# Kernel tuning notes

Measured on AMD Instinct MI355X. Metric: run time of the kernel, lower is better.

The kernel has to match this reference:

```python
import jax, jax.numpy as jnp
import numpy as np

DIM = 112        # input channels
DIM_OUT = 224    # output channels (stage transition)
HEADS = 4
HD = DIM_OUT // HEADS          # 56
WS = 8                         # window size before query pooling
QS = 2                         # query_stride
MLP_DIM = int(DIM_OUT * 4.0)   # 896
EPS = 1e-6
SCALE = HD ** -0.5


def _layernorm(x, g, b):
    m = x.mean(-1, keepdims=True)
    d = x - m
    v = (d * d).mean(-1, keepdims=True)
    return d * jax.lax.rsqrt(v + EPS) * g + b


def _maxpool2(x):
    # stride==pool_size max pooling via reshape (NHWC)
    B, H, W, C = x.shape
    return x.reshape(B, H // QS, QS, W // QS, QS, C).max(axis=(2, 4))


def setup_inputs() -> dict:
    key = jax.random.key(0)
    ks = jax.random.split(key, 8)
    def n(k, s, sc=0.02):
        return jax.random.normal(k, s, dtype=jnp.float32) * sc
    return {
        "hidden_states": jax.random.normal(ks[0], (8, 128, 128, DIM), dtype=jnp.float32),
        "ln1_g": jnp.ones((DIM,), jnp.float32),
        "ln1_b": jnp.zeros((DIM,), jnp.float32),
        "qkv_w": n(ks[1], (DIM, 3 * DIM_OUT)),
        "qkv_b": jnp.zeros((3 * DIM_OUT,), jnp.float32),
        "attn_proj_w": n(ks[2], (DIM_OUT, DIM_OUT)),
        "attn_proj_b": jnp.zeros((DIM_OUT,), jnp.float32),
        "res_proj_w": n(ks[3], (DIM, DIM_OUT)),
        "res_proj_b": jnp.zeros((DIM_OUT,), jnp.float32),
        "ln2_g": jnp.ones((DIM_OUT,), jnp.float32),
        "ln2_b": jnp.zeros((DIM_OUT,), jnp.float32),
        "mlp1_w": n(ks[4], (DIM_OUT, MLP_DIM)),
        "mlp1_b": jnp.zeros((MLP_DIM,), jnp.float32),
        "mlp2_w": n(ks[5], (MLP_DIM, DIM_OUT)),
        "mlp2_b": jnp.zeros((DIM_OUT,), jnp.float32),
    }


def reference(hidden_states, ln1_g, ln1_b, qkv_w, qkv_b, attn_proj_w, attn_proj_b,
              res_proj_w, res_proj_b, ln2_g, ln2_b, mlp1_w, mlp1_b, mlp2_w, mlp2_b):
    x = hidden_states
    B, H, W, _ = x.shape  # H, W divisible by WS -> no padding branch needed
    hs = _layernorm(x, ln1_g, ln1_b)
    # dim != dim_out: residual = pooled projection of normed input
    residual = _maxpool2(hs @ res_proj_w + res_proj_b)  # (B, H/2, W/2, DIM_OUT)

    # window partition: (B*nh*nw, WS, WS, DIM)
    nh, nw = H // WS, W // WS
    w = hs.reshape(B, nh, WS, nw, WS, DIM).transpose(0, 1, 3, 2, 4, 5)
    w = w.reshape(B * nh * nw, WS, WS, DIM)

    # multi-scale attention with query pooling
    qkv = (w @ qkv_w + qkv_b).reshape(-1, WS * WS, 3, HEADS, HD)
    q, k, v = qkv[:, :, 0], qkv[:, :, 1], qkv[:, :, 2]
    q = _maxpool2(q.reshape(-1, WS, WS, DIM_OUT))          # (Bw, WS/2, WS/2, DIM_OUT)
    q = q.reshape(-1, (WS // QS) ** 2, HEADS, HD)
    q = q.transpose(0, 2, 1, 3)   # (Bw, h, Lq, d)
    k = k.transpose(0, 2, 1, 3)   # (Bw, h, Lk, d)
    v = v.transpose(0, 2, 1, 3)
    attn = jax.nn.softmax(jnp.einsum('bhqd,bhkd->bhqk', q * SCALE, k), axis=-1)
    o = jnp.einsum('bhqk,bhkd->bhqd', attn, v).transpose(0, 2, 1, 3)
    ws2 = WS // QS
    o = o.reshape(-1, ws2, ws2, DIM_OUT)
    o = o @ attn_proj_w + attn_proj_b

    # window unpartition at pooled resolution
    H2, W2 = H // QS, W // QS
    o = o.reshape(B, nh, nw, ws2, ws2, DIM_OUT).transpose(0, 1, 3, 2, 4, 5)
    o = o.reshape(B, H2, W2, DIM_OUT)

    hs = residual + o
    ln = _layernorm(hs, ln2_g, ln2_b)
    mlp = jax.nn.gelu(ln @ mlp1_w + mlp1_b, approximate=False) @ mlp2_w + mlp2_b
    return hs + mlp
```

## Files before the change

### kernel.cpp

```cpp
#include <hip/hip_runtime.h>
#include <hip/hip_bf16.h>
#include <math.h>


#define SCALE_A 0.13363062095621219f

typedef __attribute__((ext_vector_type(8))) short short8;
typedef __attribute__((ext_vector_type(4))) short short4v;
typedef __attribute__((ext_vector_type(4))) float f32x4;
typedef __attribute__((ext_vector_type(16))) float f32x16;

__device__ inline short f2bf(float x) {
  __hip_bfloat16 h = __float2bfloat16(x);
  union { __hip_bfloat16 h; short s; } u; u.h = h;
  return u.s;
}
__device__ inline float gelu_fast(float x) {
  float x2 = x * x;
  float p = fmaf(x2, 0.044715f, 1.0f);
  float t = -1.5957691216057308f * x * p;
  return x / (1.0f + __expf(t));
}

__global__ void cast_w_kernel(const float* __restrict__ qkv_w,
                              const float* __restrict__ rp_w,
                              const float* __restrict__ ap_w,
                              const float* __restrict__ m1_w,
                              const float* __restrict__ m2_w,
                              short* __restrict__ wF) {
  int tid = blockIdx.x * blockDim.x + threadIdx.x;
  int stride = gridDim.x * blockDim.x;
  for (int e = tid; e < 90112; e += stride) {
    int j = e & 7, lr = (e >> 3) & 15, lqq = (e >> 7) & 3, tile = e >> 9;
    int kt = tile & 3, nt = tile >> 2;
    int cp = nt * 16 + lr;
    int h = cp / 176, cl = cp % 176;
    int k = kt * 32 + lqq * 8 + j;
    float val = 0.f;
    if (k < 112 && cl < 168) {
      int bcol = (cl < 56) ? (h * 56 + cl)
               : (cl < 112) ? (224 + h * 56 + (cl - 56))
                            : (448 + h * 56 + (cl - 112));
      val = qkv_w[k * 672 + bcol];
    }
    wF[e] = f2bf(val);
  }
  for (int e = tid; e < 28672; e += stride) {
    int j = e & 7, lr = (e >> 3) & 15, lqq = (e >> 7) & 3, tile = e >> 9;
    int kt = tile & 3, nt = tile >> 2;
    int n = nt * 16 + lr, k = kt * 32 + lqq * 8 + j;
    wF[90112 + e] = (k < 112) ? f2bf(rp_w[k * 224 + n]) : (short)0;
  }
  for (int e = tid; e < 50176; e += stride) {
    int j = e & 7, lr = (e >> 3) & 15, lqq = (e >> 7) & 3, tile = e >> 9;
    int kt = tile % 7, nt = tile / 7;
    int n = nt * 16 + lr, k = kt * 32 + lqq * 8 + j;
    wF[118784 + e] = f2bf(ap_w[k * 224 + n]);
  }
  for (int e = tid; e < 200704; e += stride) {
    int j = e & 7, lane = (e >> 3) & 63, unit = e >> 9;
    int kt = unit % 14, nt = unit / 14;
    int n = nt * 32 + (lane & 31), k = kt * 16 + (lane >> 5) * 8 + j;
    wF[168960 + e] = f2bf(m1_w[k * 896 + n]);
  }
  for (int e = tid; e < 200704; e += stride) {
    int j = e & 7, lane = (e >> 3) & 63, unit = e >> 9;
    int kt = unit % 56, nt = unit / 56;
    int n = nt * 32 + (lane & 31), k = kt * 16 + (lane >> 5) * 8 + j;
    wF[369664 + e] = f2bf(m2_w[k * 224 + n]);
  }
}

__global__ __launch_bounds__(256, 2) void attn_kernel(
    const float* __restrict__ x, const float* __restrict__ ln1_g,
    const float* __restrict__ ln1_b, const short* __restrict__ qkvF,
    const float* __restrict__ qkv_b, const short* __restrict__ apF,
    const float* __restrict__ apb, const short* __restrict__ rpF,
    const float* __restrict__ rpb, float* __restrict__ hs2) {
  __shared__ alignas(16) short u_s[4 * 9792];
  int win = blockIdx.x;
  int nw = win & 15, nh = (win >> 4) & 15, b = win >> 8;
  int tid = threadIdx.x;
  int wave = tid >> 6, lane = tid & 63, lrow = lane & 15, lq = lane >> 4;
  short* w_s  = u_s;
  short* k_s  = u_s + wave * 9792;
  short* vT_s = k_s + 4608;
  short* qp_s = k_s + 8640;

  {
    int part = tid & 3, m = tid >> 2;
    int p = m >> 2, r = m & 3;
    int tr = (p >> 2) * 2 + (r >> 1), tc = (p & 3) * 2 + (r & 1);
    size_t token = ((size_t)(b * 128 + nh * 8 + tr)) * 128 + (nw * 8 + tc);
    const float* xp = x + token * 112 + part * 28;
    f32x4 v[7];
    #pragma unroll
    for (int i = 0; i < 7; ++i) v[i] = *(const f32x4*)(xp + i * 4);
    float s = 0.f;
    #pragma unroll
    for (int i = 0; i < 7; ++i) s += v[i][0] + v[i][1] + v[i][2] + v[i][3];
    s += __shfl_xor(s, 1, 4);
    s += __shfl_xor(s, 2, 4);
    float mean = s * (1.f / 112.f);
    float s2 = 0.f;
    #pragma unroll
    for (int i = 0; i < 7; ++i)
      #pragma unroll
      for (int q = 0; q < 4; ++q) { float d = v[i][q] - mean; s2 = fmaf(d, d, s2); }
    s2 += __shfl_xor(s2, 1, 4);
    s2 += __shfl_xor(s2, 2, 4);
    float rs = rsqrtf(s2 * (1.f / 112.f) + 1e-6f);
    const float* gp = ln1_g + part * 28;
    const float* bp = ln1_b + part * 28;
    #pragma unroll
    for (int i = 0; i < 7; ++i) {
      f32x4 gg = *(const f32x4*)(gp + i * 4);
      f32x4 bb = *(const f32x4*)(bp + i * 4);
      short4v o;
      #pragma unroll
      for (int q = 0; q < 4; ++q)
        o[q] = f2bf((v[i][q] - mean) * rs * gg[q] + bb[q]);
      *(short4v*)&w_s[m * 136 + part * 28 + i * 4] = o;
    }
  }
  if (tid < 192) {
    short8 z = {0, 0, 0, 0, 0, 0, 0, 0};
    *(short8*)&w_s[(tid / 3) * 136 + 112 + (tid % 3) * 8] = z;
  }
  __syncthreads();

  short8 Aw[4][4];
  #pragma unroll
  for (int mt = 0; mt < 4; ++mt)
    #pragma unroll
    for (int kt = 0; kt < 4; ++kt)
      Aw[mt][kt] = *(const short8*)&w_s[(mt * 16 + lrow) * 136 + kt * 32 + lq * 8];
  __syncthreads();

  {
    short8 z = {0, 0, 0, 0, 0, 0, 0, 0};
    *(short8*)&k_s[lane * 72 + 56] = z;
    if (lane < 16) *(short8*)&qp_s[lane * 72 + 56] = z;
  }

  int h = wave;

  #pragma unroll 2
  for (int t = 0; t < 11; ++t) {
    int cl = t * 16 + lrow;
    f32x4 ac[4] = {{0.f,0.f,0.f,0.f},{0.f,0.f,0.f,0.f},
                   {0.f,0.f,0.f,0.f},{0.f,0.f,0.f,0.f}};
    short8 bw[4];
    #pragma unroll
    for (int kt = 0; kt < 4; ++kt)
      bw[kt] = *(const short8*)(qkvF + (((h * 11 + t) * 4 + kt) * 64 + lane) * 8);
    #pragma unroll
    for (int kt = 0; kt < 4; ++kt)
      #pragma unroll
      for (int mt = 0; mt < 4; ++mt)
        ac[mt] = __builtin_amdgcn_mfma_f32_16x16x32_bf16(Aw[mt][kt], bw[kt], ac[mt], 0, 0, 0);
    if (cl < 56) {
      float bias = qkv_b[h * 56 + cl];
      #pragma unroll
      for (int mt = 0; mt < 4; ++mt) {
        float mx = fmaxf(fmaxf(ac[mt][0], ac[mt][1]),
                         fmaxf(ac[mt][2], ac[mt][3])) + bias;
        qp_s[(mt * 4 + lq) * 72 + cl] = f2bf(mx * SCALE_A);
      }
    } else if (cl < 112) {
      float bias = qkv_b[224 + h * 56 + (cl - 56)];
      #pragma unroll
      for (int mt = 0; mt < 4; ++mt)
        #pragma unroll
        for (int r = 0; r < 4; ++r)
          k_s[(mt * 16 + lq * 4 + r) * 72 + (cl - 56)] = f2bf(ac[mt][r] + bias);
    } else if (cl < 168) {
      float bias = qkv_b[448 + h * 56 + (cl - 112)];
      #pragma unroll
      for (int mt = 0; mt < 4; ++mt) {
        short4v pk = {f2bf(ac[mt][0] + bias), f2bf(ac[mt][1] + bias),
                      f2bf(ac[mt][2] + bias), f2bf(ac[mt][3] + bias)};
        *(short4v*)&vT_s[(cl - 112) * 72 + mt * 16 + lq * 4] = pk;
      }
    }
  }

  short8 aq[2];
  #pragma unroll
  for (int kt = 0; kt < 2; ++kt)
    aq[kt] = *(const short8*)&qp_s[lrow * 72 + kt * 32 + lq * 8];
  f32x4 sc[4];
  #pragma unroll
  for (int t = 0; t < 4; ++t) {
    sc[t][0] = sc[t][1] = sc[t][2] = sc[t][3] = 0.f;
    #pragma unroll
    for (int kt = 0; kt < 2; ++kt) {
      short8 bk = *(const short8*)&k_s[(t * 16 + lrow) * 72 + kt * 32 + lq * 8];
      sc[t] = __builtin_amdgcn_mfma_f32_16x16x32_bf16(aq[kt], bk, sc[t], 0, 0, 0);
    }
  }
  float mr[4], sr[4];
  #pragma unroll
  for (int r = 0; r < 4; ++r)
    mr[r] = fmaxf(fmaxf(sc[0][r], sc[1][r]), fmaxf(sc[2][r], sc[3][r]));
  #pragma unroll
  for (int off = 8; off; off >>= 1)
    #pragma unroll
    for (int r = 0; r < 4; ++r) mr[r] = fmaxf(mr[r], __shfl_xor(mr[r], off, 16));
  #pragma unroll
  for (int r = 0; r < 4; ++r) {
    #pragma unroll
    for (int t = 0; t < 4; ++t) sc[t][r] = __expf(sc[t][r] - mr[r]);
    sr[r] = sc[0][r] + sc[1][r] + sc[2][r] + sc[3][r];
  }
  #pragma unroll
  for (int off = 8; off; off >>= 1)
    #pragma unroll
    for (int r = 0; r < 4; ++r) sr[r] += __shfl_xor(sr[r], off, 16);
  #pragma unroll
  for (int r = 0; r < 4; ++r) sr[r] = 1.f / sr[r];
  #pragma unroll
  for (int t = 0; t < 4; ++t)
    #pragma unroll
    for (int r = 0; r < 4; ++r)
      qp_s[(lq * 4 + r) * 72 + t * 16 + lrow] = f2bf(sc[t][r] * sr[r]);

  short8 ap[2];
  #pragma unroll
  for (int kt = 0; kt < 2; ++kt)
    ap[kt] = *(const short8*)&qp_s[lrow * 72 + kt * 32 + lq * 8];
  #pragma unroll
  for (int ct = 0; ct < 4; ++ct) {
    int c0 = (ct < 3) ? ct * 16 : 40;
    int col = c0 + lrow;
    f32x4 ov = {0.f, 0.f, 0.f, 0.f};
    #pragma unroll
    for (int kt = 0; kt < 2; ++kt) {
      short8 bv = *(const short8*)&vT_s[col * 72 + kt * 32 + lq * 8];
      ov = __builtin_amdgcn_mfma_f32_16x16x32_bf16(ap[kt], bv, ov, 0, 0, 0);
    }
    if (ct < 3 || lrow >= 8) {
      #pragma unroll
      for (int r = 0; r < 4; ++r)
        qp_s[(lq * 4 + r) * 72 + col] = f2bf(ov[r]);
    }
  }

  int nt0 = (wave < 2) ? wave * 4 : 8 + (wave - 2) * 3;
  int ncnt2 = (wave < 2) ? 4 : 3;
  float resv[4][4];
  #pragma unroll
  for (int i = 0; i < 4; ++i) {
    if (i < ncnt2) {
      int nt = nt0 + i;
      f32x4 racc[4] = {{0.f,0.f,0.f,0.f},{0.f,0.f,0.f,0.f},
                       {0.f,0.f,0.f,0.f},{0.f,0.f,0.f,0.f}};
      short8 rw[4];
      #pragma unroll
      for (int kt = 0; kt < 4; ++kt)
        rw[kt] = *(const short8*)(rpF + (((nt * 4) + kt) * 64 + lane) * 8);
      #pragma unroll
      for (int kt = 0; kt < 4; ++kt)
        #pragma unroll
        for (int mt = 0; mt < 4; ++mt)
          racc[mt] = __builtin_amdgcn_mfma_f32_16x16x32_bf16(Aw[mt][kt], rw[kt], racc[mt], 0, 0, 0);
      float bi = rpb[nt * 16 + lrow];
      #pragma unroll
      for (int mt = 0; mt < 4; ++mt)
        resv[i][mt] = fmaxf(fmaxf(racc[mt][0], racc[mt][1]),
                            fmaxf(racc[mt][2], racc[mt][3])) + bi;
    }
  }
  __syncthreads();

  float* res_s = (float*)u_s;
  #pragma unroll
  for (int i = 0; i < 4; ++i) {
    if (i < ncnt2) {
      int nt = nt0 + i;
      #pragma unroll
      for (int mt = 0; mt < 4; ++mt)
        res_s[(mt * 4 + lq) * 228 + nt * 16 + lrow] = resv[i][mt];
    }
  }

  short8 Ao[7];
  #pragma unroll
  for (int kt = 0; kt < 7; ++kt) {
    int c = kt * 32 + lq * 8;
    int h2 = (c >= 168) ? 3 : (c >= 112) ? 2 : (c >= 56) ? 1 : 0;
    Ao[kt] = *(const short8*)&u_s[h2 * 9792 + 8640 + lrow * 72 + (c - h2 * 56)];
  }
  for (int i = 0; i < ncnt2; ++i) {
    int nt = nt0 + i;
    f32x4 acc = {0.f, 0.f, 0.f, 0.f};
    #pragma unroll
    for (int kt = 0; kt < 7; ++kt) {
      short8 bw = *(const short8*)(apF + ((nt * 7 + kt) * 64 + lane) * 8);
      acc = __builtin_amdgcn_mfma_f32_16x16x32_bf16(Ao[kt], bw, acc, 0, 0, 0);
    }
    int col2 = nt * 16 + lrow;
    float bi = apb[col2];
    #pragma unroll
    for (int r = 0; r < 4; ++r) {
      float res = res_s[(lq * 4 + r) * 228 + col2];
      size_t token = ((size_t)(b * 64 + nh * 4 + lq)) * 64 + nw * 4 + r;
      hs2[token * 224 + col2] = res + acc[r] + bi;
    }
  }
}

template <int NT>
__device__ __forceinline__ void mlp1_tiles(
    int nt0, const short* ln_s, const short* __restrict__ m1F,
    const float* __restrict__ b1, short* hid_s, int nl, int half, int lane) {
  f32x16 acc[NT];
  #pragma unroll
  for (int i = 0; i < NT; ++i)
    #pragma unroll
    for (int r = 0; r < 16; ++r) acc[i][r] = 0.f;
  #pragma unroll
  for (int kt = 0; kt < 14; ++kt) {
    short8 a = *(const short8*)&ln_s[nl * 232 + kt * 16 + half * 8];
    #pragma unroll
    for (int i = 0; i < NT; ++i) {
      short8 bw = *(const short8*)(m1F + ((size_t)((nt0 + i) * 14 + kt) * 64 + lane) * 8);
      acc[i] = __builtin_amdgcn_mfma_f32_32x32x16_bf16(a, bw, acc[i], 0, 0, 0);
    }
  }
  #pragma unroll
  for (int i = 0; i < NT; ++i) {
    int col = (nt0 + i) * 32 + nl;
    float bi = b1[col];
    #pragma unroll
    for (int r = 0; r < 16; ++r) {
      int row = (r & 3) + 8 * (r >> 2) + 4 * half;
      hid_s[row * 904 + col] = f2bf(gelu_fast(acc[i][r] + bi));
    }
  }
}

__global__ __launch_bounds__(512, 4) void mlp_kernel(
    const float* __restrict__ hs2, const float* __restrict__ g2,
    const float* __restrict__ b2, const short* __restrict__ m1F,
    const float* __restrict__ b1, const short* __restrict__ m2F,
    const float* __restrict__ b2b, float* __restrict__ out) {
  __shared__ alignas(16) short ln_s[32 * 232];
  __shared__ alignas(16) short hid_s[32 * 904];
  int blk = blockIdx.x;
  int tid = threadIdx.x;
  size_t base = (size_t)blk * 32 * 224;
  {
    int row = tid >> 4, l = tid & 15;
    const float* rp = hs2 + base + (size_t)row * 224 + l * 14;
    float v[14];
    float s = 0.f;
    #pragma unroll
    for (int c = 0; c < 7; ++c) {
      float2 t = *(const float2*)(rp + 2 * c);
      v[2 * c] = t.x; v[2 * c + 1] = t.y;
      s += t.x + t.y;
    }
    #pragma unroll
    for (int off = 8; off; off >>= 1) s += __shfl_xor(s, off, 16);
    float mean = s * (1.f / 224.f);
    float s2 = 0.f;
    #pragma unroll
    for (int c = 0; c < 14; ++c) { float d = v[c] - mean; s2 = fmaf(d, d, s2); }
    #pragma unroll
    for (int off = 8; off; off >>= 1) s2 += __shfl_xor(s2, off, 16);
    float rs = rsqrtf(s2 * (1.f / 224.f) + 1e-6f);
    const float* gp = g2 + l * 14;
    const float* bp = b2 + l * 14;
    #pragma unroll
    for (int c = 0; c < 7; ++c) {
      float2 gg = *(const float2*)(gp + 2 * c);
      float2 bb = *(const float2*)(bp + 2 * c);
      unsigned lo = (unsigned short)f2bf((v[2 * c] - mean) * rs * gg.x + bb.x);
      unsigned hi = (unsigned short)f2bf((v[2 * c + 1] - mean) * rs * gg.y + bb.y);
      *(unsigned*)&ln_s[row * 232 + l * 14 + 2 * c] = lo | (hi << 16);
    }
  }
  __syncthreads();
  int wave = tid >> 6, lane = tid & 63;
  int nl = lane & 31, half = lane >> 5;
  if (wave < 4) mlp1_tiles<4>(wave * 4, ln_s, m1F, b1, hid_s, nl, half, lane);
  else          mlp1_tiles<3>(16 + (wave - 4) * 3, ln_s, m1F, b1, hid_s, nl, half, lane);
  __syncthreads();
  if (wave < 7) {
    int nt = wave;
    int col = nt * 32 + nl;
    float res[16];
    #pragma unroll
    for (int r = 0; r < 16; ++r) {
      int row = (r & 3) + 8 * (r >> 2) + 4 * half;
      res[r] = hs2[base + (size_t)row * 224 + col];
    }
    f32x16 ac0 = {0.f,0.f,0.f,0.f,0.f,0.f,0.f,0.f,0.f,0.f,0.f,0.f,0.f,0.f,0.f,0.f};
    f32x16 ac1 = {0.f,0.f,0.f,0.f,0.f,0.f,0.f,0.f,0.f,0.f,0.f,0.f,0.f,0.f,0.f,0.f};
    #pragma unroll 4
    for (int kt = 0; kt < 56; kt += 2) {
      short8 a0 = *(const short8*)&hid_s[nl * 904 + kt * 16 + half * 8];
      short8 a1 = *(const short8*)&hid_s[nl * 904 + (kt + 1) * 16 + half * 8];
      short8 b0 = *(const short8*)(m2F + ((size_t)(nt * 56 + kt) * 64 + lane) * 8);
      short8 b1 = *(const short8*)(m2F + ((size_t)(nt * 56 + kt + 1) * 64 + lane) * 8);
      ac0 = __builtin_amdgcn_mfma_f32_32x32x16_bf16(a0, b0, ac0, 0, 0, 0);
      ac1 = __builtin_amdgcn_mfma_f32_32x32x16_bf16(a1, b1, ac1, 0, 0, 0);
    }
    float bi = b2b[col];
    #pragma unroll
    for (int r = 0; r < 16; ++r) {
      int row = (r & 3) + 8 * (r >> 2) + 4 * half;
      size_t idx = base + (size_t)row * 224 + col;
      out[idx] = res[r] + ac0[r] + ac1[r] + bi;
    }
  }
}

extern "C" void kernel_launch(void* const* d_in, const int* in_sizes, int n_in,
                              void* d_out, int out_size, void* d_ws, size_t ws_size,
                              hipStream_t stream) {
  const float* x    = (const float*)d_in[0];
  const float* ln1g = (const float*)d_in[1];
  const float* ln1b = (const float*)d_in[2];
  const float* qkvw = (const float*)d_in[3];
  const float* qkvb = (const float*)d_in[4];
  const float* apw  = (const float*)d_in[5];
  const float* apb  = (const float*)d_in[6];
  const float* rpw  = (const float*)d_in[7];
  const float* rpb  = (const float*)d_in[8];
  const float* ln2g = (const float*)d_in[9];
  const float* ln2b = (const float*)d_in[10];
  const float* w1   = (const float*)d_in[11];
  const float* b1   = (const float*)d_in[12];
  const float* w2   = (const float*)d_in[13];
  const float* b2   = (const float*)d_in[14];
  float* out = (float*)d_out;

  float* hs2 = (float*)((char*)d_ws + 29360128);
  short* wF  = (short*)((char*)d_ws + 73400320);

  cast_w_kernel<<<1024, 256, 0, stream>>>(qkvw, rpw, apw, w1, w2, wF);
  attn_kernel<<<2048, 256, 0, stream>>>(x, ln1g, ln1b, wF, qkvb, wF + 118784,
                                        apb, wF + 90112, rpb, hs2);
  mlp_kernel<<<1024, 512, 0, stream>>>(hs2, ln2g, ln2b, wF + 168960, b1,
                                       wF + 369664, b2, out);
}
```

Baseline: 213.7 us.

## Switch MLP kernel to 16-row blocks with 16x16x32 MFMA tiles

The MLP kernel now handles 16 tokens per block with 256 threads instead of 32 tokens with 512 threads, and uses 16x16x32 bf16 MFMAs in place of 32x32x16. The weight pre-layout for mlp1 and mlp2 is changed to match the 16x16x32 fragment layout. All four waves now do work in the second GEMM (4/4/3/3 column tiles each), where before one of eight waves sat idle. Each weight fragment is reused across half as many rows, so global and L2 weight traffic per token roughly doubles, in exchange for smaller LDS use, more blocks and better wave balance.

```diff
diff --git a/kernel.cpp b/kernel.cpp
--- a/kernel.cpp
+++ b/kernel.cpp
@@ -58,15 +58,15 @@
     wF[118784 + e] = f2bf(ap_w[k * 224 + n]);
   }
   for (int e = tid; e < 200704; e += stride) {
-    int j = e & 7, lane = (e >> 3) & 63, unit = e >> 9;
-    int kt = unit % 14, nt = unit / 14;
-    int n = nt * 32 + (lane & 31), k = kt * 16 + (lane >> 5) * 8 + j;
+    int j = e & 7, lr = (e >> 3) & 15, lqq = (e >> 7) & 3, tile = e >> 9;
+    int kt = tile % 7, nt = tile / 7;
+    int n = nt * 16 + lr, k = kt * 32 + lqq * 8 + j;
     wF[168960 + e] = f2bf(m1_w[k * 896 + n]);
   }
   for (int e = tid; e < 200704; e += stride) {
-    int j = e & 7, lane = (e >> 3) & 63, unit = e >> 9;
-    int kt = unit % 56, nt = unit / 56;
-    int n = nt * 32 + (lane & 31), k = kt * 16 + (lane >> 5) * 8 + j;
+    int j = e & 7, lr = (e >> 3) & 15, lqq = (e >> 7) & 3, tile = e >> 9;
+    int kt = tile % 28, nt = tile / 28;
+    int n = nt * 16 + lr, k = kt * 32 + lqq * 8 + j;
     wF[369664 + e] = f2bf(m2_w[k * 224 + n]);
   }
 }
@@ -310,46 +310,41 @@
   }
 }
 
-template <int NT>
-__device__ __forceinline__ void mlp1_tiles(
+__device__ __forceinline__ void mlp1_g7(
     int nt0, const short* ln_s, const short* __restrict__ m1F,
-    const float* __restrict__ b1, short* hid_s, int nl, int half, int lane) {
-  f32x16 acc[NT];
-  #pragma unroll
-  for (int i = 0; i < NT; ++i)
-    #pragma unroll
-    for (int r = 0; r < 16; ++r) acc[i][r] = 0.f;
-  #pragma unroll
-  for (int kt = 0; kt < 14; ++kt) {
-    short8 a = *(const short8*)&ln_s[nl * 232 + kt * 16 + half * 8];
-    #pragma unroll
-    for (int i = 0; i < NT; ++i) {
-      short8 bw = *(const short8*)(m1F + ((size_t)((nt0 + i) * 14 + kt) * 64 + lane) * 8);
-      acc[i] = __builtin_amdgcn_mfma_f32_32x32x16_bf16(a, bw, acc[i], 0, 0, 0);
-    }
-  }
-  #pragma unroll
-  for (int i = 0; i < NT; ++i) {
-    int col = (nt0 + i) * 32 + nl;
+    const float* __restrict__ b1, short* hid_s, int lrow, int lq, int lane) {
+  f32x4 acc[7];
+  #pragma unroll
+  for (int i = 0; i < 7; ++i) { acc[i][0] = acc[i][1] = acc[i][2] = acc[i][3] = 0.f; }
+  #pragma unroll
+  for (int kt = 0; kt < 7; ++kt) {
+    short8 a = *(const short8*)&ln_s[lrow * 232 + kt * 32 + lq * 8];
+    #pragma unroll
+    for (int i = 0; i < 7; ++i) {
+      short8 bw = *(const short8*)(m1F + ((size_t)((nt0 + i) * 7 + kt) * 64 + lane) * 8);
+      acc[i] = __builtin_amdgcn_mfma_f32_16x16x32_bf16(a, bw, acc[i], 0, 0, 0);
+    }
+  }
+  #pragma unroll
+  for (int i = 0; i < 7; ++i) {
+    int col = (nt0 + i) * 16 + lrow;
     float bi = b1[col];
     #pragma unroll
-    for (int r = 0; r < 16; ++r) {
-      int row = (r & 3) + 8 * (r >> 2) + 4 * half;
-      hid_s[row * 904 + col] = f2bf(gelu_fast(acc[i][r] + bi));
-    }
-  }
-}
-
-__global__ __launch_bounds__(512, 4) void mlp_kernel(
+    for (int r = 0; r < 4; ++r)
+      hid_s[(lq * 4 + r) * 904 + col] = f2bf(gelu_fast(acc[i][r] + bi));
+  }
+}
+
+__global__ __launch_bounds__(256, 4) void mlp_kernel(
     const float* __restrict__ hs2, const float* __restrict__ g2,
     const float* __restrict__ b2, const short* __restrict__ m1F,
     const float* __restrict__ b1, const short* __restrict__ m2F,
     const float* __restrict__ b2b, float* __restrict__ out) {
-  __shared__ alignas(16) short ln_s[32 * 232];
-  __shared__ alignas(16) short hid_s[32 * 904];
+  __shared__ alignas(16) short ln_s[16 * 232];
+  __shared__ alignas(16) short hid_s[16 * 904];
   int blk = blockIdx.x;
   int tid = threadIdx.x;
-  size_t base = (size_t)blk * 32 * 224;
+  size_t base = (size_t)blk * 16 * 224;
   {
     int row = tid >> 4, l = tid & 15;
     const float* rp = hs2 + base + (size_t)row * 224 + l * 14;
@@ -383,36 +378,46 @@
   }
   __syncthreads();
   int wave = tid >> 6, lane = tid & 63;
-  int nl = lane & 31, half = lane >> 5;
-  if (wave < 4) mlp1_tiles<4>(wave * 4, ln_s, m1F, b1, hid_s, nl, half, lane);
-  else          mlp1_tiles<3>(16 + (wave - 4) * 3, ln_s, m1F, b1, hid_s, nl, half, lane);
+  int lrow = lane & 15, lq = lane >> 4;
+  mlp1_g7(wave * 14, ln_s, m1F, b1, hid_s, lrow, lq, lane);
+  mlp1_g7(wave * 14 + 7, ln_s, m1F, b1, hid_s, lrow, lq, lane);
   __syncthreads();
-  if (wave < 7) {
-    int nt = wave;
-    int col = nt * 32 + nl;
-    float res[16];
-    #pragma unroll
-    for (int r = 0; r < 16; ++r) {
-      int row = (r & 3) + 8 * (r >> 2) + 4 * half;
-      res[r] = hs2[base + (size_t)row * 224 + col];
-    }
-    f32x16 ac0 = {0.f,0.f,0.f,0.f,0.f,0.f,0.f,0.f,0.f,0.f,0.f,0.f,0.f,0.f,0.f,0.f};
-    f32x16 ac1 = {0.f,0.f,0.f,0.f,0.f,0.f,0.f,0.f,0.f,0.f,0.f,0.f,0.f,0.f,0.f,0.f};
-    #pragma unroll 4
-    for (int kt = 0; kt < 56; kt += 2) {
-      short8 a0 = *(const short8*)&hid_s[nl * 904 + kt * 16 + half * 8];
-      short8 a1 = *(const short8*)&hid_s[nl * 904 + (kt + 1) * 16 + half * 8];
-      short8 b0 = *(const short8*)(m2F + ((size_t)(nt * 56 + kt) * 64 + lane) * 8);
-      short8 b1 = *(const short8*)(m2F + ((size_t)(nt * 56 + kt + 1) * 64 + lane) * 8);
-      ac0 = __builtin_amdgcn_mfma_f32_32x32x16_bf16(a0, b0, ac0, 0, 0, 0);
-      ac1 = __builtin_amdgcn_mfma_f32_32x32x16_bf16(a1, b1, ac1, 0, 0, 0);
-    }
-    float bi = b2b[col];
-    #pragma unroll
-    for (int r = 0; r < 16; ++r) {
-      int row = (r & 3) + 8 * (r >> 2) + 4 * half;
-      size_t idx = base + (size_t)row * 224 + col;
-      out[idx] = res[r] + ac0[r] + ac1[r] + bi;
+  int nt0 = (wave < 2) ? wave * 4 : 8 + (wave - 2) * 3;
+  int cnt = (wave < 2) ? 4 : 3;
+  float res[4][4];
+  #pragma unroll
+  for (int i = 0; i < 4; ++i) {
+    if (i < cnt) {
+      int col = (nt0 + i) * 16 + lrow;
+      #pragma unroll
+      for (int r = 0; r < 4; ++r)
+        res[i][r] = hs2[base + (size_t)(lq * 4 + r) * 224 + col];
+    }
+  }
+  f32x4 ac[4];
+  #pragma unroll
+  for (int i = 0; i < 4; ++i) { ac[i][0] = ac[i][1] = ac[i][2] = ac[i][3] = 0.f; }
+  #pragma unroll 4
+  for (int kt = 0; kt < 28; ++kt) {
+    short8 a = *(const short8*)&hid_s[lrow * 904 + kt * 32 + lq * 8];
+    #pragma unroll
+    for (int i = 0; i < 4; ++i) {
+      if (i < cnt) {
+        short8 bw = *(const short8*)(m2F + ((size_t)((nt0 + i) * 28 + kt) * 64 + lane) * 8);
+        ac[i] = __builtin_amdgcn_mfma_f32_16x16x32_bf16(a, bw, ac[i], 0, 0, 0);
+      }
+    }
+  }
+  #pragma unroll
+  for (int i = 0; i < 4; ++i) {
+    if (i < cnt) {
+      int col = (nt0 + i) * 16 + lrow;
+      float bi = b2b[col];
+      #pragma unroll
+      for (int r = 0; r < 4; ++r) {
+        size_t idx = base + (size_t)(lq * 4 + r) * 224 + col;
+        out[idx] = res[i][r] + ac[i][r] + bi;
+      }
     }
   }
 }
@@ -443,6 +448,6 @@
   cast_w_kernel<<<1024, 256, 0, stream>>>(qkvw, rpw, apw, w1, w2, wF);
   attn_kernel<<<2048, 256, 0, stream>>>(x, ln1g, ln1b, wF, qkvb, wF + 118784,
                                         apb, wF + 90112, rpb, hs2);
-  mlp_kernel<<<1024, 512, 0, stream>>>(hs2, ln2g, ln2b, wF + 168960, b1,
+  mlp_kernel<<<2048, 256, 0, stream>>>(hs2, ln2g, ln2b, wF + 168960, b1,
                                        wF + 369664, b2, out);
 }
```

New measurement: 246.5 us. 1.15x slower.
